# Kernel tuning notes

Hardware: AMD Instinct MI355X
Metric: run time of the kernel (lower is better)

The kernel has to match this reference:

```python
import jax, jax.numpy as jnp
import numpy as np

N = 50000   # nodes
E = 200000  # edges per relation
R = 4       # relations
IN = 128
HID = 32
H = 4
OUT = 32


def setup_inputs() -> dict:
    key = jax.random.key(0)
    ks = jax.random.split(key, 32)
    w = lambda k, shape: jax.random.normal(k, shape, jnp.float32) * 0.05
    inp = {
        "x": jax.random.normal(ks[0], (N, IN), jnp.float32),
        "edge_src": jax.random.randint(ks[1], (R, E), 0, N, dtype=jnp.int32),
        "edge_dst": jax.random.randint(ks[2], (R, E), 0, N, dtype=jnp.int32),
    }
    # (d_in, heads*d_out, d_out) per layer: flatten, flatten, mean-over-heads
    dims = [(IN, H * HID, HID), (H * HID, H * HID, HID), (H * HID, H * OUT, OUT)]
    i = 3
    for l, (din, dout, d) in enumerate(dims):
        inp[f"Wsrc{l}"] = w(ks[i], (R, din, dout)); i += 1
        inp[f"bsrc{l}"] = w(ks[i], (R, dout)); i += 1
        inp[f"Wdst{l}"] = w(ks[i], (R, din, dout)); i += 1
        inp[f"bdst{l}"] = w(ks[i], (R, dout)); i += 1
        inp[f"attn{l}"] = w(ks[i], (R, H, d)); i += 1
    return inp


def rel_gatv2(h, src, dst, Ws, bs, Wd, bd, att):
    """DGL GATv2Conv for one relation: gather, leaky-relu score, edge softmax, scatter-sum."""
    n = h.shape[0]
    heads, d = att.shape
    fs = (h @ Ws + bs).reshape(n, heads, d)   # [N,H,D]
    fd = (h @ Wd + bd).reshape(n, heads, d)
    e = jax.nn.leaky_relu(fs[src] + fd[dst], 0.2)        # [E,H,D]
    score = jnp.einsum('ehd,hd->eh', e, att)             # [E,H]
    # numerically stable edge softmax segmented by destination node
    m = jax.lax.stop_gradient(jax.ops.segment_max(score, dst, num_segments=n))
    m = jnp.where(jnp.isfinite(m), m, 0.0)               # zero-in-degree guard
    ex = jnp.exp(score - m[dst])
    den = jax.ops.segment_sum(ex, dst, num_segments=n)
    a = ex / jnp.maximum(den[dst], 1e-16)                # [E,H]
    return jax.ops.segment_sum(a[:, :, None] * fs[src], dst, num_segments=n)  # [N,H,D]


def gat_layer(h, edge_src, edge_dst, Ws, bs, Wd, bd, att, mean_heads):
    out = None
    for r in range(Ws.shape[0]):  # small fixed relation count; HeteroGraphConv sums
        o = rel_gatv2(h, edge_src[r], edge_dst[r], Ws[r], bs[r], Wd[r], bd[r], att[r])
        out = o if out is None else out + o
    if mean_heads:                # last_layer_flag: mean over heads
        return out.mean(axis=1)
    return out.reshape(h.shape[0], -1)  # flatten heads


def reference(x, edge_src, edge_dst,
              Wsrc0, bsrc0, Wdst0, bdst0, attn0,
              Wsrc1, bsrc1, Wdst1, bdst1, attn1,
              Wsrc2, bsrc2, Wdst2, bdst2, attn2):
    h = gat_layer(x, edge_src, edge_dst, Wsrc0, bsrc0, Wdst0, bdst0, attn0, False)
    h = gat_layer(h, edge_src, edge_dst, Wsrc1, bsrc1, Wdst1, bdst1, attn1, False)
    h = gat_layer(h, edge_src, edge_dst, Wsrc2, bsrc2, Wdst2, bdst2, attn2, True)
    return h  # [N, OUT]
```

## Files before the change

### kernel.cpp

```cpp
#include <hip/hip_runtime.h>
#include <math.h>

#define FF 128
#define CAP 32
#define GB 512

typedef _Float16 half2v __attribute__((ext_vector_type(2)));
typedef _Float16 f16x8  __attribute__((ext_vector_type(8)));
typedef __fp16   fp16x2 __attribute__((ext_vector_type(2)));
typedef __attribute__((ext_vector_type(4))) float f4v;

__device__ __forceinline__ half2v u2h(unsigned u) {
    union { unsigned u; half2v h; } c; c.u = u; return c.h;
}
__device__ __forceinline__ unsigned h2u(half2v h) {
    union { unsigned u; half2v h; } c; c.h = h; return c.u;
}
__device__ __forceinline__ unsigned short f2h(float f) {
    _Float16 h = (_Float16)f;
    unsigned short u; __builtin_memcpy(&u, &h, 2); return u;
}
__device__ __forceinline__ half2v pk2h(float e) {
    union { fp16x2 p; half2v h; } c;
    c.p = __builtin_amdgcn_cvt_pkrtz(e, e);
    return c.h;
}
__device__ __forceinline__ float dot2(half2v a, half2v b, float c) {
#if __has_builtin(__builtin_amdgcn_fdot2)
    union { half2v h; fp16x2 p; } ca, cb;
    ca.h = a; cb.h = b;
    return __builtin_amdgcn_fdot2(ca.p, cb.p, c, false);
#else
    return c + (float)a.x * (float)b.x + (float)a.y * (float)b.y;
#endif
}
__device__ __forceinline__ half2v shfladd_h(half2v v, int mask) {
    return v + u2h(__shfl_xor(h2u(v), mask));
}

__global__ __launch_bounds__(256, 2) void setup_fused(
    const float* __restrict__ x,
    const float* __restrict__ W0s_, const float* __restrict__ bs0,
    const float* __restrict__ W0d_, const float* __restrict__ bd0,
    unsigned short* __restrict__ fs_all, unsigned short* __restrict__ fd_all,
    int nrb, int n,
    const int* __restrict__ esrc_all, const int* __restrict__ edst_all,
    int* __restrict__ cursor, int* __restrict__ slots, int totalE, int ne,
    const float* __restrict__ W1s_, const float* __restrict__ W1d_,
    const float* __restrict__ W2s_, const float* __restrict__ W2d_,
    unsigned short* __restrict__ Wp,
    const float* __restrict__ a0, const float* __restrict__ a1,
    const float* __restrict__ a2, unsigned* __restrict__ attH,
    int CB)
{
    const int tid = threadIdx.x;
    int role, b;
    if (blockIdx.x < 2 * GB) {
        role = blockIdx.x & 1;
        b = blockIdx.x >> 1;
    } else {
        int rest = blockIdx.x - 2 * GB;
        const int csrRest = CB - GB;
        if (rest < csrRest) { role = 1; b = GB + rest; }
        else {
            rest -= csrRest;
            if (rest < 1536) { role = 2; b = rest; }
            else             { role = 3; b = rest - 1536; }
        }
    }

    if (role == 0) {
        const int wave = tid >> 6, lane = tid & 63;
        const int r = b & 3;
        const int half = wave & 1;
        const int lo = lane & 15, quad = lane >> 4;

        unsigned short* fs = fs_all + (size_t)r * n * FF;
        unsigned short* fd = fd_all + (size_t)r * n * FF;

        f16x8 B[2][4][4];
        #pragma unroll
        for (int mat = 0; mat < 2; ++mat) {
            const float* W = (mat == 0) ? W0s_ : W0d_;
            #pragma unroll
            for (int nbi = 0; nbi < 4; ++nbi)
                #pragma unroll
                for (int ks = 0; ks < 4; ++ks) {
                    const int nn = (half * 4 + nbi) * 16 + lo;
                    f16x8 v;
                    #pragma unroll
                    for (int j = 0; j < 8; ++j) {
                        const int k = ks * 32 + quad * 8 + j;
                        v[j] = (_Float16)W[((size_t)r * FF + k) * FF + nn];
                    }
                    B[mat][nbi][ks] = v;
                }
        }

        float biasS[4], biasD[4];
        #pragma unroll
        for (int nbi = 0; nbi < 4; ++nbi) {
            biasS[nbi] = bs0[r * FF + (half * 4 + nbi) * 16 + lo];
            biasD[nbi] = bd0[r * FF + (half * 4 + nbi) * 16 + lo];
        }

        const int stride = (GB >> 2) * 2;
        for (int rb = (b >> 2) * 2 + (wave >> 1); rb < nrb; rb += stride) {
            const int row0 = rb * 16;
            f16x8 A[4];
            #pragma unroll
            for (int ks = 0; ks < 4; ++ks) {
                const float* ap = &x[(size_t)(row0 + lo) * FF + ks * 32 + quad * 8];
                const float4 p0 = *(const float4*)&ap[0];
                const float4 p1 = *(const float4*)&ap[4];
                f16x8 v;
                v[0] = (_Float16)p0.x; v[1] = (_Float16)p0.y;
                v[2] = (_Float16)p0.z; v[3] = (_Float16)p0.w;
                v[4] = (_Float16)p1.x; v[5] = (_Float16)p1.y;
                v[6] = (_Float16)p1.z; v[7] = (_Float16)p1.w;
                A[ks] = v;
            }

            f4v cS[4], cD[4];
            #pragma unroll
            for (int nbi = 0; nbi < 4; ++nbi) {
                cS[nbi] = (f4v){biasS[nbi], biasS[nbi], biasS[nbi], biasS[nbi]};
                cD[nbi] = (f4v){biasD[nbi], biasD[nbi], biasD[nbi], biasD[nbi]};
            }

            #pragma unroll
            for (int ks = 0; ks < 4; ++ks)
                #pragma unroll
                for (int nbi = 0; nbi < 4; ++nbi) {
                    cS[nbi] = __builtin_amdgcn_mfma_f32_16x16x32_f16(
                        A[ks], B[0][nbi][ks], cS[nbi], 0, 0, 0);
                    cD[nbi] = __builtin_amdgcn_mfma_f32_16x16x32_f16(
                        A[ks], B[1][nbi][ks], cD[nbi], 0, 0, 0);
                }

            #pragma unroll
            for (int nbi = 0; nbi < 4; ++nbi)
                #pragma unroll
                for (int i = 0; i < 4; ++i) {
                    const size_t o = (size_t)(row0 + quad * 4 + i) * FF
                                   + (half * 4 + nbi) * 16 + lo;
                    fs[o] = f2h(cS[nbi][i]);
                    fd[o] = f2h(cD[nbi][i]);
                }
        }
        return;
    }

    if (role == 1) {
        const int t0 = b * 1024 + tid;
        #pragma unroll
        for (int k = 0; k < 4; ++k) {
            const int i = t0 + k * 256;
            if (i < totalE) {
                const int r = i / ne;
                const int rd = r * n + edst_all[i];
                const int idx = atomicAdd(&cursor[rd], 1);
                slots[(size_t)rd * CAP + idx] = esrc_all[i];
            }
        }
        return;
    }

    if (role == 2) {
        const int t = b * 256 + tid;
        if (t >= 3 * 4 * 2 * FF * FF) return;
        const int l    = t >> 17;
        const int rest = t & 131071;
        const int r    = rest >> 15;
        const int mat  = (rest >> 14) & 1;
        const int idx  = rest & 16383;
        const int k = idx >> 7, nn = idx & 127;
        const float* W = (l == 0) ? (mat ? W0d_ : W0s_)
                       : (l == 1) ? (mat ? W1d_ : W1s_)
                                  : (mat ? W2d_ : W2s_);
        const float v = W[((size_t)r * FF + k) * FF + nn];
        const int nb = nn >> 4, lo = nn & 15;
        const int ks = k >> 5, quad = (k >> 3) & 3, j = k & 7;
        const int lane = quad * 16 + lo;
        const size_t o = (((((((size_t)l * 4 + r) * 2 + mat) * 8 + nb) * 4 + ks) * 64 + lane) * 8) + j;
        Wp[o] = f2h(v);
        return;
    }

    const int t = b * 256 + tid;
    if (t >= 768) return;
    const int l = t >> 8, rest = t & 255;
    const float* a = (l == 0) ? a0 : (l == 1) ? a1 : a2;
    const float2 v = ((const float2*)a)[rest];
    half2v h = {(_Float16)v.x, (_Float16)v.y};
    attH[t] = h2u(h);
}

__global__ __launch_bounds__(256, 2) void mfma_gemm(
    const unsigned short* __restrict__ hb,
    const unsigned short* __restrict__ Wp,
    const float* __restrict__ bs_all,
    const float* __restrict__ bd_all,
    unsigned short* __restrict__ fs_all,
    unsigned short* __restrict__ fd_all,
    int nrb, int n)
{
    const int wave = threadIdx.x >> 6, lane = threadIdx.x & 63;
    const int r = blockIdx.x & 3;
    const int half = wave & 1;
    const int lo = lane & 15, quad = lane >> 4;

    const unsigned short* Wr = Wp + (size_t)r * 2 * FF * FF;
    unsigned short* fs = fs_all + (size_t)r * n * FF;
    unsigned short* fd = fd_all + (size_t)r * n * FF;

    f16x8 B[2][4][4];
    #pragma unroll
    for (int mat = 0; mat < 2; ++mat)
        #pragma unroll
        for (int nbi = 0; nbi < 4; ++nbi)
            #pragma unroll
            for (int ks = 0; ks < 4; ++ks) {
                const int nb = half * 4 + nbi;
                B[mat][nbi][ks] = *(const f16x8*)
                    &Wr[(((((size_t)mat * 8 + nb) * 4 + ks) * 64 + lane) * 8)];
            }

    float biasS[4], biasD[4];
    #pragma unroll
    for (int nbi = 0; nbi < 4; ++nbi) {
        biasS[nbi] = bs_all[r * FF + (half * 4 + nbi) * 16 + lo];
        biasD[nbi] = bd_all[r * FF + (half * 4 + nbi) * 16 + lo];
    }

    const int stride = (gridDim.x >> 2) * 2;
    for (int rb = (blockIdx.x >> 2) * 2 + (wave >> 1); rb < nrb; rb += stride) {
        const int row0 = rb * 16;
        f16x8 A[4];
        #pragma unroll
        for (int ks = 0; ks < 4; ++ks)
            A[ks] = *(const f16x8*)&hb[(size_t)(row0 + lo) * FF + ks * 32 + quad * 8];

        f4v cS[4], cD[4];
        #pragma unroll
        for (int nbi = 0; nbi < 4; ++nbi) {
            cS[nbi] = (f4v){biasS[nbi], biasS[nbi], biasS[nbi], biasS[nbi]};
            cD[nbi] = (f4v){biasD[nbi], biasD[nbi], biasD[nbi], biasD[nbi]};
        }

        #pragma unroll
        for (int ks = 0; ks < 4; ++ks)
            #pragma unroll
            for (int nbi = 0; nbi < 4; ++nbi) {
                cS[nbi] = __builtin_amdgcn_mfma_f32_16x16x32_f16(
                    A[ks], B[0][nbi][ks], cS[nbi], 0, 0, 0);
                cD[nbi] = __builtin_amdgcn_mfma_f32_16x16x32_f16(
                    A[ks], B[1][nbi][ks], cD[nbi], 0, 0, 0);
            }

        #pragma unroll
        for (int nbi = 0; nbi < 4; ++nbi)
            #pragma unroll
            for (int i = 0; i < 4; ++i) {
                const size_t o = (size_t)(row0 + quad * 4 + i) * FF
                               + (half * 4 + nbi) * 16 + lo;
                fs[o] = f2h(cS[nbi][i]);
                fd[o] = f2h(cD[nbi][i]);
            }
    }
}

__device__ __forceinline__ void edge4(
    uint4 g, bool ok, const half2v* fdv, const half2v* atv,
    float& den, half2v* acc)
{
    const half2v C02 = {(_Float16)0.2f, (_Float16)0.2f};
    half2v f[4] = {u2h(g.x), u2h(g.y), u2h(g.z), u2h(g.w)};
    float v = 0.f;
    #pragma unroll
    for (int i = 0; i < 4; ++i) {
        const half2v z = f[i] + fdv[i];
        const half2v l = __builtin_elementwise_max(z, z * C02);
        v = dot2(l, atv[i], v);
    }
    v += __shfl_xor(v, 2);
    v += __shfl_xor(v, 1);
    const float e = ok ? __expf(v) : 0.f;
    den += e;
    const half2v eh = pk2h(e);
    #pragma unroll
    for (int i = 0; i < 4; ++i) acc[i] += eh * f[i];
}

__global__ __launch_bounds__(256) void aggregate(
    const int* __restrict__ cnt,
    const int* __restrict__ slots,
    const unsigned* __restrict__ fs_all,
    const unsigned* __restrict__ fd_all,
    const unsigned* __restrict__ att_h,
    unsigned* __restrict__ out_h,
    float* __restrict__ out_f32,
    int n)
{
    const int node = blockIdx.x * 4 + (threadIdx.x >> 6);
    if (node >= n) return;
    const int lane = threadIdx.x & 63;
    const int quarter = lane >> 4;
    const int q = lane & 15;
    const int fo = 4 * q;

    int m[4]; int4 sA[4];
    #pragma unroll
    for (int r = 0; r < 4; ++r) {
        const size_t rd = (size_t)r * n + node;
        m[r]  = cnt[rd];
        sA[r] = *(const int4*)&slots[rd * CAP];
    }

    half2v val[4];
    #pragma unroll
    for (int i = 0; i < 4; ++i) val[i] = (half2v){(_Float16)0.f, (_Float16)0.f};

    #pragma unroll
    for (int r = 0; r < 4; ++r) {
        const int mr = m[r];
        if (mr == 0) continue;
        const size_t rd = (size_t)r * n + node;
        const unsigned* fsu = fs_all + (size_t)r * n * 64;

        const int4 sB = *(const int4*)&slots[rd * CAP + 4];
        const uint4 ufd = *(const uint4*)&fd_all[rd * 64 + fo];
        const uint4 uat = *(const uint4*)&att_h[r * 64 + fo];
        half2v fdv[4] = {u2h(ufd.x), u2h(ufd.y), u2h(ufd.z), u2h(ufd.w)};
        half2v atv[4] = {u2h(uat.x), u2h(uat.y), u2h(uat.z), u2h(uat.w)};

        const bool ok0 = quarter < mr;
        const bool ok1 = 4 + quarter < mr;
        int i0 = (quarter == 0) ? sA[r].x : (quarter == 1) ? sA[r].y
               : (quarter == 2) ? sA[r].z : sA[r].w;
        int i1 = (quarter == 0) ? sB.x : (quarter == 1) ? sB.y
               : (quarter == 2) ? sB.z : sB.w;
        i0 = ok0 ? i0 : 0;
        i1 = ok1 ? i1 : 0;
        const uint4 g0 = *(const uint4*)&fsu[(size_t)i0 * 64 + fo];
        const uint4 g1 = *(const uint4*)&fsu[(size_t)i1 * 64 + fo];

        float den = 0.f;
        half2v acc[4];
        #pragma unroll
        for (int i = 0; i < 4; ++i) acc[i] = (half2v){(_Float16)0.f, (_Float16)0.f};

        edge4(g0, ok0, fdv, atv, den, acc);
        if (mr > 4)
            edge4(g1, ok1, fdv, atv, den, acc);

        if (mr > 8) {
            const int* sl = slots + rd * CAP;
            for (int p = 8; p < mr; p += 4) {
                const int ei = p + quarter;
                const bool ok = ei < mr;
                int s = sl[ei < CAP ? ei : CAP - 1]; s = ok ? s : 0;
                const uint4 g = *(const uint4*)&fsu[(size_t)s * 64 + fo];
                edge4(g, ok, fdv, atv, den, acc);
            }
        }

        den += __shfl_xor(den, 16);
        den += __shfl_xor(den, 32);
        const half2v ih = pk2h(__builtin_amdgcn_rcpf(den));
        #pragma unroll
        for (int i = 0; i < 4; ++i) val[i] += acc[i] * ih;
    }

    #pragma unroll
    for (int i = 0; i < 4; ++i) {
        val[i] = shfladd_h(val[i], 16);
        val[i] = shfladd_h(val[i], 32);
    }

    if (out_f32) {
        #pragma unroll
        for (int i = 0; i < 4; ++i) {
            val[i] = shfladd_h(val[i], 4);
            val[i] = shfladd_h(val[i], 8);
        }
        if (lane < 4) {
            float* o = &out_f32[(size_t)node * 32 + 8 * lane];
            *(float4*)&o[0] = make_float4(0.25f * (float)val[0].x, 0.25f * (float)val[0].y,
                                          0.25f * (float)val[1].x, 0.25f * (float)val[1].y);
            *(float4*)&o[4] = make_float4(0.25f * (float)val[2].x, 0.25f * (float)val[2].y,
                                          0.25f * (float)val[3].x, 0.25f * (float)val[3].y);
        }
    } else {
        if (lane < 16) {
            uint4 o;
            o.x = h2u(val[0]); o.y = h2u(val[1]);
            o.z = h2u(val[2]); o.w = h2u(val[3]);
            *(uint4*)&out_h[(size_t)node * 64 + fo] = o;
        }
    }
}

extern "C" void kernel_launch(void* const* d_in, const int* in_sizes, int n_in,
                              void* d_out, int out_size, void* d_ws, size_t ws_size,
                              hipStream_t stream)
{
    const int n  = in_sizes[0] / FF;
    const int R  = 4;
    const int ne = in_sizes[1] / R;
    const int totalE = R * ne;
    const int L  = R * n;
    const int nrb = (n + 15) / 16;

    const float* x    = (const float*)d_in[0];
    const int*   esrc = (const int*)d_in[1];
    const int*   edst = (const int*)d_in[2];

    char* p = (char*)d_ws;
    auto carve = [&p](size_t bytes) { char* q = p; p += (bytes + 255) & ~(size_t)255; return q; };
    unsigned*       hbA    = (unsigned*)      carve((size_t)n * 64 * 4);
    unsigned*       hbB    = (unsigned*)      carve((size_t)n * 64 * 4);
    unsigned short* fs_all = (unsigned short*)carve((size_t)R * n * FF * 2);
    unsigned short* fd_all = (unsigned short*)carve((size_t)R * n * FF * 2);
    unsigned short* Wp     = (unsigned short*)carve((size_t)3 * R * 2 * FF * FF * 2);
    unsigned*       attH   = (unsigned*)      carve((size_t)3 * R * 64 * 4);
    int*            cursor = (int*)           carve((size_t)L * 4);
    int*            slots  = (int*)           carve((size_t)L * CAP * 4);

    (void)hipMemsetAsync(cursor, 0, (size_t)L * sizeof(int), stream);

    const int CB = (totalE + 1023) / 1024;
    setup_fused<<<2 * GB + (CB - GB) + 1536 + 3, 256, 0, stream>>>(
        x,
        (const float*)d_in[3], (const float*)d_in[4],
        (const float*)d_in[5], (const float*)d_in[6],
        fs_all, fd_all, nrb, n,
        esrc, edst, cursor, slots, totalE, ne,
        (const float*)d_in[8],  (const float*)d_in[10],
        (const float*)d_in[13], (const float*)d_in[15],
        Wp,
        (const float*)d_in[7], (const float*)d_in[12], (const float*)d_in[17],
        attH, CB);

    unsigned* bufs[3] = {hbA, hbB, nullptr};
    for (int l = 0; l < 3; ++l) {
        if (l > 0) {
            const float* bsrc = (const float*)d_in[3 + 5 * l + 1];
            const float* bdst = (const float*)d_in[3 + 5 * l + 3];
            mfma_gemm<<<512, 256, 0, stream>>>(
                (const unsigned short*)bufs[l - 1],
                Wp + (size_t)l * R * 2 * FF * FF,
                bsrc, bdst, fs_all, fd_all, nrb, n);
        }
        const int last = (l == 2);
        aggregate<<<(n + 3) / 4, 256, 0, stream>>>(
            cursor, slots,
            (const unsigned*)fs_all, (const unsigned*)fd_all,
            attH + (size_t)l * R * 64,
            last ? nullptr : bufs[l],
            last ? (float*)d_out : nullptr, n);
    }
}
```

Baseline: 432.0 us.

## Process relations in pairs to overlap gathers; simplify setup block role mapping

The aggregation kernel now handles two relations at once, issuing their slot, fd, attention and first gather loads together so more memory requests are in flight per wave before the edge math runs. Separately, setup_fused drops the interleaved GEMM/CSR block assignment in favour of contiguous ranges: GEMM blocks first, then CSR, weight packing and attention conversion. The pairing raises register pressure and does some loads for relations with zero in-degree. The new setup ordering removes the overlap between GEMM and atomic CSR-building blocks, which could change load balance.

```diff
diff --git a/kernel.cpp b/kernel.cpp
--- a/kernel.cpp
+++ b/kernel.cpp
@@ -36,6 +36,10 @@
 }
 __device__ __forceinline__ half2v shfladd_h(half2v v, int mask) {
     return v + u2h(__shfl_xor(h2u(v), mask));
+}
+__device__ __forceinline__ int qsel(int4 v, int quarter) {
+    return (quarter == 0) ? v.x : (quarter == 1) ? v.y
+         : (quarter == 2) ? v.z : v.w;
 }
 
 __global__ __launch_bounds__(256, 2) void setup_fused(
@@ -53,23 +57,10 @@
     const float* __restrict__ a2, unsigned* __restrict__ attH,
     int CB)
 {
+    int b = blockIdx.x;
     const int tid = threadIdx.x;
-    int role, b;
-    if (blockIdx.x < 2 * GB) {
-        role = blockIdx.x & 1;
-        b = blockIdx.x >> 1;
-    } else {
-        int rest = blockIdx.x - 2 * GB;
-        const int csrRest = CB - GB;
-        if (rest < csrRest) { role = 1; b = GB + rest; }
-        else {
-            rest -= csrRest;
-            if (rest < 1536) { role = 2; b = rest; }
-            else             { role = 3; b = rest - 1536; }
-        }
-    }
-
-    if (role == 0) {
+
+    if (b < GB) {
         const int wave = tid >> 6, lane = tid & 63;
         const int r = b & 3;
         const int half = wave & 1;
@@ -150,8 +141,9 @@
         }
         return;
     }
-
-    if (role == 1) {
+    b -= GB;
+
+    if (b < CB) {
         const int t0 = b * 1024 + tid;
         #pragma unroll
         for (int k = 0; k < 4; ++k) {
@@ -165,8 +157,9 @@
         }
         return;
     }
-
-    if (role == 2) {
+    b -= CB;
+
+    if (b < 1536) {
         const int t = b * 256 + tid;
         if (t >= 3 * 4 * 2 * FF * FF) return;
         const int l    = t >> 17;
@@ -186,6 +179,7 @@
         Wp[o] = f2h(v);
         return;
     }
+    b -= 1536;
 
     const int t = b * 256 + tid;
     if (t >= 768) return;
@@ -322,54 +316,85 @@
     for (int i = 0; i < 4; ++i) val[i] = (half2v){(_Float16)0.f, (_Float16)0.f};
 
     #pragma unroll
-    for (int r = 0; r < 4; ++r) {
-        const int mr = m[r];
-        if (mr == 0) continue;
-        const size_t rd = (size_t)r * n + node;
-        const unsigned* fsu = fs_all + (size_t)r * n * 64;
-
-        const int4 sB = *(const int4*)&slots[rd * CAP + 4];
-        const uint4 ufd = *(const uint4*)&fd_all[rd * 64 + fo];
-        const uint4 uat = *(const uint4*)&att_h[r * 64 + fo];
-        half2v fdv[4] = {u2h(ufd.x), u2h(ufd.y), u2h(ufd.z), u2h(ufd.w)};
-        half2v atv[4] = {u2h(uat.x), u2h(uat.y), u2h(uat.z), u2h(uat.w)};
-
-        const bool ok0 = quarter < mr;
-        const bool ok1 = 4 + quarter < mr;
-        int i0 = (quarter == 0) ? sA[r].x : (quarter == 1) ? sA[r].y
-               : (quarter == 2) ? sA[r].z : sA[r].w;
-        int i1 = (quarter == 0) ? sB.x : (quarter == 1) ? sB.y
-               : (quarter == 2) ? sB.z : sB.w;
-        i0 = ok0 ? i0 : 0;
-        i1 = ok1 ? i1 : 0;
-        const uint4 g0 = *(const uint4*)&fsu[(size_t)i0 * 64 + fo];
-        const uint4 g1 = *(const uint4*)&fsu[(size_t)i1 * 64 + fo];
-
-        float den = 0.f;
-        half2v acc[4];
-        #pragma unroll
-        for (int i = 0; i < 4; ++i) acc[i] = (half2v){(_Float16)0.f, (_Float16)0.f};
-
-        edge4(g0, ok0, fdv, atv, den, acc);
-        if (mr > 4)
-            edge4(g1, ok1, fdv, atv, den, acc);
-
-        if (mr > 8) {
-            const int* sl = slots + rd * CAP;
-            for (int p = 8; p < mr; p += 4) {
+    for (int rp = 0; rp < 2; ++rp) {
+        const int ra = 2 * rp, rb = 2 * rp + 1;
+        const size_t rdA = (size_t)ra * n + node;
+        const size_t rdB = (size_t)rb * n + node;
+        const int mA = m[ra], mB = m[rb];
+        const unsigned* fsuA = fs_all + (size_t)ra * n * 64;
+        const unsigned* fsuB = fs_all + (size_t)rb * n * 64;
+
+        const int4 sBA = *(const int4*)&slots[rdA * CAP + 4];
+        const int4 sBB = *(const int4*)&slots[rdB * CAP + 4];
+        const uint4 ufdA = *(const uint4*)&fd_all[rdA * 64 + fo];
+        const uint4 ufdB = *(const uint4*)&fd_all[rdB * 64 + fo];
+        const uint4 uatA = *(const uint4*)&att_h[ra * 64 + fo];
+        const uint4 uatB = *(const uint4*)&att_h[rb * 64 + fo];
+
+        const bool okA0 = quarter < mA, okA1 = 4 + quarter < mA;
+        const bool okB0 = quarter < mB, okB1 = 4 + quarter < mB;
+        int iA0 = qsel(sA[ra], quarter); iA0 = okA0 ? iA0 : 0;
+        int iB0 = qsel(sA[rb], quarter); iB0 = okB0 ? iB0 : 0;
+        int iA1 = qsel(sBA, quarter);    iA1 = okA1 ? iA1 : 0;
+        int iB1 = qsel(sBB, quarter);    iB1 = okB1 ? iB1 : 0;
+        const uint4 gA0 = *(const uint4*)&fsuA[(size_t)iA0 * 64 + fo];
+        const uint4 gB0 = *(const uint4*)&fsuB[(size_t)iB0 * 64 + fo];
+        const uint4 gA1 = *(const uint4*)&fsuA[(size_t)iA1 * 64 + fo];
+        const uint4 gB1 = *(const uint4*)&fsuB[(size_t)iB1 * 64 + fo];
+
+        half2v fdvA[4] = {u2h(ufdA.x), u2h(ufdA.y), u2h(ufdA.z), u2h(ufdA.w)};
+        half2v atvA[4] = {u2h(uatA.x), u2h(uatA.y), u2h(uatA.z), u2h(uatA.w)};
+        half2v fdvB[4] = {u2h(ufdB.x), u2h(ufdB.y), u2h(ufdB.z), u2h(ufdB.w)};
+        half2v atvB[4] = {u2h(uatB.x), u2h(uatB.y), u2h(uatB.z), u2h(uatB.w)};
+
+        float denA = 0.f, denB = 0.f;
+        half2v accA[4], accB[4];
+        #pragma unroll
+        for (int i = 0; i < 4; ++i) {
+            accA[i] = (half2v){(_Float16)0.f, (_Float16)0.f};
+            accB[i] = (half2v){(_Float16)0.f, (_Float16)0.f};
+        }
+
+        edge4(gA0, okA0, fdvA, atvA, denA, accA);
+        edge4(gB0, okB0, fdvB, atvB, denB, accB);
+        if (mA > 4) edge4(gA1, okA1, fdvA, atvA, denA, accA);
+        if (mB > 4) edge4(gB1, okB1, fdvB, atvB, denB, accB);
+
+        if (mA > 8) {
+            const int* sl = slots + rdA * CAP;
+            for (int p = 8; p < mA; p += 4) {
                 const int ei = p + quarter;
-                const bool ok = ei < mr;
+                const bool ok = ei < mA;
                 int s = sl[ei < CAP ? ei : CAP - 1]; s = ok ? s : 0;
-                const uint4 g = *(const uint4*)&fsu[(size_t)s * 64 + fo];
-                edge4(g, ok, fdv, atv, den, acc);
-            }
-        }
-
-        den += __shfl_xor(den, 16);
-        den += __shfl_xor(den, 32);
-        const half2v ih = pk2h(__builtin_amdgcn_rcpf(den));
-        #pragma unroll
-        for (int i = 0; i < 4; ++i) val[i] += acc[i] * ih;
+                const uint4 g = *(const uint4*)&fsuA[(size_t)s * 64 + fo];
+                edge4(g, ok, fdvA, atvA, denA, accA);
+            }
+        }
+        if (mB > 8) {
+            const int* sl = slots + rdB * CAP;
+            for (int p = 8; p < mB; p += 4) {
+                const int ei = p + quarter;
+                const bool ok = ei < mB;
+                int s = sl[ei < CAP ? ei : CAP - 1]; s = ok ? s : 0;
+                const uint4 g = *(const uint4*)&fsuB[(size_t)s * 64 + fo];
+                edge4(g, ok, fdvB, atvB, denB, accB);
+            }
+        }
+
+        if (mA) {
+            denA += __shfl_xor(denA, 16);
+            denA += __shfl_xor(denA, 32);
+            const half2v ih = pk2h(__builtin_amdgcn_rcpf(denA));
+            #pragma unroll
+            for (int i = 0; i < 4; ++i) val[i] += accA[i] * ih;
+        }
+        if (mB) {
+            denB += __shfl_xor(denB, 16);
+            denB += __shfl_xor(denB, 32);
+            const half2v ih = pk2h(__builtin_amdgcn_rcpf(denB));
+            #pragma unroll
+            for (int i = 0; i < 4; ++i) val[i] += accB[i] * ih;
+        }
     }
 
     #pragma unroll
@@ -430,7 +455,7 @@
     (void)hipMemsetAsync(cursor, 0, (size_t)L * sizeof(int), stream);
 
     const int CB = (totalE + 1023) / 1024;
-    setup_fused<<<2 * GB + (CB - GB) + 1536 + 3, 256, 0, stream>>>(
+    setup_fused<<<GB + CB + 1536 + 3, 256, 0, stream>>>(
         x,
         (const float*)d_in[3], (const float*)d_in[4],
         (const float*)d_in[5], (const float*)d_in[6],
```

Result: faster. 421.6 us (median of 2 runs) (-2.4%).
